# Kernel tuning notes

Hardware: AMD Instinct MI355X
Metric: run time of the kernel (lower is better)

The kernel has to match this reference:

```python
import jax, jax.numpy as jnp
import numpy as np

B, N, EN, C, F, HEADS, DE = 2, 8192, 16, 256, 512, 8, 8
D = C // HEADS  # att_size = 32
TAU = 0.1


def _xavier(k, shape):
    lim = float(np.sqrt(6.0 / (shape[0] + shape[1])))
    return jax.random.uniform(k, shape, jnp.float32, -lim, lim)


def setup_inputs() -> dict:
    key = jax.random.key(0)
    ks = jax.random.split(key, 16)
    return {
        "xyz": jax.random.normal(ks[0], (B, N, 3), jnp.float32),
        "features": jax.random.normal(ks[1], (B, C, N), jnp.float32),
        "edges": jax.random.randint(ks[2], (B, N * EN, 2), 0, N),
        "gumbel_u": jax.random.uniform(ks[3], (B * N, DE, EN), jnp.float32, 1e-6, 1.0 - 1e-6),
        "g1": jnp.ones((C,), jnp.float32), "be1": jnp.zeros((C,), jnp.float32),
        "Wq": _xavier(ks[4], (C, C)),
        "Wk": _xavier(ks[5], (C + 3, C)),
        "Wv": _xavier(ks[6], (C + 3, C)),
        "Wo": _xavier(ks[7], (C, C)),
        "g2": jnp.ones((C,), jnp.float32), "be2": jnp.zeros((C,), jnp.float32),
        "W1": _xavier(ks[8], (C, F)), "bf1": jnp.zeros((F,), jnp.float32),
        "W2": _xavier(ks[9], (F, C)), "bf2": jnp.zeros((C,), jnp.float32),
        "D1": _xavier(ks[10], (C, C // 2)), "db1": jnp.zeros((C // 2,), jnp.float32),
        "D2": _xavier(ks[11], (C // 2, DE)), "db2": jnp.zeros((DE,), jnp.float32),
    }


def _ln(x, g, b):
    m = jnp.mean(x, -1, keepdims=True)
    v = jnp.mean((x - m) ** 2, -1, keepdims=True)
    return (x - m) * jax.lax.rsqrt(v + 1e-6) * g + b


def reference(xyz, features, edges, gumbel_u, g1, be1, Wq, Wk, Wv, Wo,
              g2, be2, W1, bf1, W2, bf2, D1, db1, D2, db2):
    feats = jnp.transpose(features, (0, 2, 1))            # b,n,C
    x = _ln(feats, g1, be1)
    idx = edges[:, :, 0]                                  # b, n*EN (neighbor ids)
    gather = jax.vmap(lambda a, i: a[i])
    sf = gather(x, idx).reshape(B, N, EN, C)              # neighbor features
    sc = gather(xyz, idx).reshape(B, N, EN, 3)            # neighbor coords
    # learned gumbel-softmax downsample: EN -> DE edges per node
    sf2 = sf.reshape(B * N, EN, C)
    h = jax.nn.relu(sf2 @ D1 + db1) @ D2 + db2            # (B*N, EN, DE)
    logits = jnp.transpose(h, (0, 2, 1))                  # (B*N, DE, EN)
    gnoise = -jnp.log(-jnp.log(gumbel_u))
    w = jax.nn.softmax((logits + gnoise) / TAU, axis=-1)
    sf = jnp.einsum('bde,bec->bdc', w, sf2).reshape(B, N, DE, C)
    sc = jnp.einsum('bde,bec->bdc', w, sc.reshape(B * N, EN, 3)).reshape(B, N, DE, 3)
    s = jnp.concatenate([sf, sc - xyz[:, :, None, :]], axis=-1)  # b,n,DE,C+3
    # local neighbor multi-head attention
    k = (s @ Wk).reshape(B, N, DE, HEADS, D)
    v = (s @ Wv).reshape(B, N, DE, HEADS, D)
    q = (x @ Wq).reshape(B, N, HEADS, D)
    simi = jnp.einsum('bnehd,bnhd->bneh', k, q) * (1.0 / float(np.sqrt(D)))
    sm = jax.nn.softmax(simi, axis=2)                     # over neighbor axis
    o = jnp.einsum('bnehd,bneh->bnhd', v, sm).reshape(B, N, C) @ Wo
    feats = feats + o
    y = _ln(feats, g2, be2)
    y = jax.nn.relu(y @ W1 + bf1) @ W2 + bf2
    feats = feats + y
    return jnp.transpose(feats, (0, 2, 1))
```

## Files before the change

### kernel.cpp

```cpp
#include <hip/hip_runtime.h>
#include <math.h>

#define NB 8192
#define CC 256

using bf16x8 = __attribute__((ext_vector_type(8))) short;
using f32x4  = __attribute__((ext_vector_type(4))) float;

__device__ inline ushort f2b(float f) {
  union { float f; unsigned u; } v; v.f = f;
  unsigned u = v.u;
  u += 0x7FFF + ((u >> 16) & 1);
  return (ushort)(u >> 16);
}
__device__ inline float b2f(ushort h) {
  union { unsigned u; float f; } v; v.u = ((unsigned)h) << 16; return v.f;
}
__device__ inline float u2f(unsigned u) {
  union { unsigned u; float f; } v; v.u = u; return v.f;
}

__global__ __launch_bounds__(256) void wpackT(const float* __restrict__ Wk, const float* __restrict__ Wv,
                                              const float* __restrict__ Wq, const float* __restrict__ Wo,
                                              const float* __restrict__ W1, const float* __restrict__ W2,
                                              const float* __restrict__ D1,
                                              ushort* __restrict__ WtKVQ, ushort* __restrict__ WtO,
                                              ushort* __restrict__ Wt1, ushort* __restrict__ Wt2,
                                              ushort* __restrict__ D1hi, ushort* __restrict__ D1lo) {
  int i = blockIdx.x * 256 + threadIdx.x;
  if (i < 196608) {
    int n = i >> 8, k = i & 255;
    float v = (n < 256) ? Wk[(size_t)k * 256 + n]
            : (n < 512) ? Wv[(size_t)k * 256 + (n - 256)]
                        : Wq[(size_t)k * 256 + (n - 512)];
    WtKVQ[(size_t)n * 256 + k] = f2b(v);
  } else if (i < 262144) {
    int j = i - 196608; int n = j >> 8, k = j & 255;
    WtO[(size_t)n * 256 + k] = f2b(Wo[(size_t)k * 256 + n]);
  } else if (i < 393216) {
    int j = i - 262144; int n = j >> 8, k = j & 255;
    Wt1[(size_t)n * 256 + k] = f2b(W1[(size_t)k * 512 + n]);
  } else if (i < 524288) {
    int j = i - 393216; int n = j >> 9, k = j & 511;
    Wt2[(size_t)n * 512 + k] = f2b(W2[(size_t)k * 256 + n]);
  } else if (i < 557056) {
    int j = i - 524288; int n = j >> 8, k = j & 255;
    D1hi[(size_t)n * 256 + k] = f2b(D1[(size_t)k * 128 + n]);
  } else {
    int j = i - 557056; int n = j >> 8, k = j & 255;
    float v = D1[(size_t)k * 128 + n];
    ushort hi = f2b(v);
    D1lo[(size_t)n * 256 + k] = f2b(v - b2f(hi));
  }
}

__global__ __launch_bounds__(256) void k1_ln1(const float* __restrict__ features,
                                              const float* __restrict__ g1,
                                              const float* __restrict__ be1,
                                              float* __restrict__ X,
                                              float* __restrict__ F) {
  __shared__ float tile[256][36];
  int b = blockIdx.y;
  int n0 = blockIdx.x * 32;
  int t = threadIdx.x;
  int tn = t & 31, ch = t >> 5;
  for (int cb = 0; cb < 32; ++cb) {
    int c = cb * 8 + ch;
    tile[c][tn] = features[((size_t)b * 256 + c) * NB + n0 + tn];
  }
  __syncthreads();
  int tok = t >> 3, sub = t & 7;
  float s = 0.f, ss = 0.f;
  #pragma unroll
  for (int k = 0; k < 32; ++k) {
    float v = tile[sub + 8 * k][tok];
    s += v; ss += v * v;
  }
  #pragma unroll
  for (int m = 1; m < 8; m <<= 1) { s += __shfl_xor(s, m); ss += __shfl_xor(ss, m); }
  float mean = s * (1.f / 256.f);
  float var  = ss * (1.f / 256.f) - mean * mean;
  float rstd = rsqrtf(var + 1e-6f);
  size_t row = ((size_t)b * NB + n0 + tok) * 256;
  for (int k = 0; k < 32; ++k) {
    int c = sub + 8 * k;
    float v = tile[c][tok];
    F[row + c] = v;
    X[row + c] = (v - mean) * rstd * g1[c] + be1[c];
  }
}

__global__ __launch_bounds__(256) void gemm_mfma_x2(
    const float* __restrict__ A, int lda,
    const ushort* __restrict__ Bhi, const ushort* __restrict__ Blo,
    float* __restrict__ Cc, int ldc, int K,
    const float* __restrict__ bias)
{
  __shared__ __align__(16) ushort Ah[128 * 32], Al[128 * 32], Bh[128 * 32], Bl[128 * 32];
  int t = threadIdx.x;
  int m0 = blockIdx.y * 128;
  int wv = t >> 6, lane = t & 63;
  int wm = wv >> 1, wn = wv & 1;
  int lr = lane & 15, kg = lane >> 4;
  f32x4 acc[4][4];
  #pragma unroll
  for (int i = 0; i < 4; ++i)
    #pragma unroll
    for (int j = 0; j < 4; ++j) acc[i][j] = (f32x4)0.0f;

  for (int k0 = 0; k0 < K; k0 += 32) {
    #pragma unroll
    for (int p = 0; p < 2; ++p) {
      int c = t + p * 256;
      int m = c >> 2, kq = c & 3;
      const float* src = &A[(size_t)(m0 + m) * lda + k0 + kq * 8];
      float v[8];
      *(float4*)&v[0] = *(const float4*)src;
      *(float4*)&v[4] = *(const float4*)(src + 4);
      ushort hi[8], lo[8];
      #pragma unroll
      for (int j = 0; j < 8; ++j) {
        hi[j] = f2b(v[j]);
        lo[j] = f2b(v[j] - b2f(hi[j]));
      }
      int off = m * 32 + (kq ^ ((m >> 1) & 3)) * 8;
      *(uint4*)&Ah[off] = *(uint4*)hi;
      *(uint4*)&Al[off] = *(uint4*)lo;
    }
    #pragma unroll
    for (int p = 0; p < 2; ++p) {
      int c = t + p * 256;
      int n = c >> 2, kq = c & 3;
      int off = n * 32 + (kq ^ ((n >> 1) & 3)) * 8;
      *(uint4*)&Bh[off] = *(const uint4*)&Bhi[(size_t)n * K + k0 + kq * 8];
      *(uint4*)&Bl[off] = *(const uint4*)&Blo[(size_t)n * K + k0 + kq * 8];
    }
    __syncthreads();
    bf16x8 ahi[4], alo[4], bhi[4], blo[4];
    #pragma unroll
    for (int mi = 0; mi < 4; ++mi) {
      int m = wm * 64 + mi * 16 + lr;
      int off = m * 32 + (kg ^ ((m >> 1) & 3)) * 8;
      ahi[mi] = *(const bf16x8*)&Ah[off];
      alo[mi] = *(const bf16x8*)&Al[off];
    }
    #pragma unroll
    for (int ni = 0; ni < 4; ++ni) {
      int n = wn * 64 + ni * 16 + lr;
      int off = n * 32 + (kg ^ ((n >> 1) & 3)) * 8;
      bhi[ni] = *(const bf16x8*)&Bh[off];
      blo[ni] = *(const bf16x8*)&Bl[off];
    }
    #pragma unroll
    for (int mi = 0; mi < 4; ++mi)
      #pragma unroll
      for (int ni = 0; ni < 4; ++ni) {
        acc[mi][ni] = __builtin_amdgcn_mfma_f32_16x16x32_bf16(ahi[mi], bhi[ni], acc[mi][ni], 0, 0, 0);
        acc[mi][ni] = __builtin_amdgcn_mfma_f32_16x16x32_bf16(ahi[mi], blo[ni], acc[mi][ni], 0, 0, 0);
        acc[mi][ni] = __builtin_amdgcn_mfma_f32_16x16x32_bf16(alo[mi], bhi[ni], acc[mi][ni], 0, 0, 0);
      }
    __syncthreads();
  }
  #pragma unroll
  for (int ni = 0; ni < 4; ++ni) {
    int col = wn * 64 + ni * 16 + lr;
    float bv = bias[col];
    #pragma unroll
    for (int mi = 0; mi < 4; ++mi)
      #pragma unroll
      for (int r = 0; r < 4; ++r) {
        int row = m0 + wm * 64 + mi * 16 + kg * 4 + r;
        Cc[(size_t)row * ldc + col] = acc[mi][ni][r] + bv;
      }
  }
}

__global__ __launch_bounds__(256) void gemm_mfma(
    const float* __restrict__ A, int lda,
    const ushort* __restrict__ Bt,
    float* __restrict__ Cc, int ldc,
    int K,
    const float* __restrict__ bias, int relu,
    const float* __restrict__ resid, int ldr,
    const float* __restrict__ mrs, const float* __restrict__ lg, const float* __restrict__ lb)
{
  __shared__ __align__(16) ushort As[128 * 32];
  __shared__ __align__(16) ushort Bs[128 * 32];
  int t = threadIdx.x;
  int m0 = blockIdx.y * 128, n0 = blockIdx.x * 128;
  int wv = t >> 6, lane = t & 63;
  int wm = wv >> 1, wn = wv & 1;
  int lr = lane & 15, kg = lane >> 4;
  f32x4 acc[4][4];
  #pragma unroll
  for (int i = 0; i < 4; ++i)
    #pragma unroll
    for (int j = 0; j < 4; ++j) acc[i][j] = (f32x4)0.0f;

  for (int k0 = 0; k0 < K; k0 += 32) {
    #pragma unroll
    for (int p = 0; p < 2; ++p) {
      int c = t + p * 256;
      int m = c >> 2, kq = c & 3;
      const float* src = &A[(size_t)(m0 + m) * lda + k0 + kq * 8];
      float v[8];
      *(float4*)&v[0] = *(const float4*)src;
      *(float4*)&v[4] = *(const float4*)(src + 4);
      if (mrs) {
        float mean = mrs[(m0 + m) * 2], rstd = mrs[(m0 + m) * 2 + 1];
        #pragma unroll
        for (int j = 0; j < 8; ++j) {
          int kk = k0 + kq * 8 + j;
          v[j] = (v[j] - mean) * rstd * lg[kk] + lb[kk];
        }
      }
      ushort o[8];
      #pragma unroll
      for (int j = 0; j < 8; ++j) o[j] = f2b(v[j]);
      *(uint4*)&As[m * 32 + (kq ^ ((m >> 1) & 3)) * 8] = *(uint4*)o;
    }
    #pragma unroll
    for (int p = 0; p < 2; ++p) {
      int c = t + p * 256;
      int n = c >> 2, kq = c & 3;
      uint4 w = *(const uint4*)&Bt[(size_t)(n0 + n) * K + k0 + kq * 8];
      *(uint4*)&Bs[n * 32 + (kq ^ ((n >> 1) & 3)) * 8] = w;
    }
    __syncthreads();
    bf16x8 af[4], bfr[4];
    #pragma unroll
    for (int mi = 0; mi < 4; ++mi) {
      int m = wm * 64 + mi * 16 + lr;
      af[mi] = *(const bf16x8*)&As[m * 32 + (kg ^ ((m >> 1) & 3)) * 8];
    }
    #pragma unroll
    for (int ni = 0; ni < 4; ++ni) {
      int n = wn * 64 + ni * 16 + lr;
      bfr[ni] = *(const bf16x8*)&Bs[n * 32 + (kg ^ ((n >> 1) & 3)) * 8];
    }
    #pragma unroll
    for (int mi = 0; mi < 4; ++mi)
      #pragma unroll
      for (int ni = 0; ni < 4; ++ni)
        acc[mi][ni] = __builtin_amdgcn_mfma_f32_16x16x32_bf16(af[mi], bfr[ni], acc[mi][ni], 0, 0, 0);
    __syncthreads();
  }
  #pragma unroll
  for (int ni = 0; ni < 4; ++ni) {
    int col = n0 + wn * 64 + ni * 16 + lr;
    float bv = bias ? bias[col] : 0.f;
    #pragma unroll
    for (int mi = 0; mi < 4; ++mi) {
      #pragma unroll
      for (int r = 0; r < 4; ++r) {
        int row = m0 + wm * 64 + mi * 16 + kg * 4 + r;
        float v = acc[mi][ni][r] + bv;
        if (relu) v = fmaxf(v, 0.f);
        if (resid) v += resid[(size_t)row * ldr + col];
        Cc[(size_t)row * ldc + col] = v;
      }
    }
  }
}

__global__ __launch_bounds__(256) void gemm_mfma_b16o(
    const float* __restrict__ A, int lda,
    const ushort* __restrict__ Bt,
    ushort* __restrict__ Cc, int ldc, int K)
{
  __shared__ __align__(16) ushort As[128 * 32];
  __shared__ __align__(16) ushort Bs[128 * 32];
  int t = threadIdx.x;
  int m0 = blockIdx.y * 128, n0 = blockIdx.x * 128;
  int wv = t >> 6, lane = t & 63;
  int wm = wv >> 1, wn = wv & 1;
  int lr = lane & 15, kg = lane >> 4;
  f32x4 acc[4][4];
  #pragma unroll
  for (int i = 0; i < 4; ++i)
    #pragma unroll
    for (int j = 0; j < 4; ++j) acc[i][j] = (f32x4)0.0f;

  for (int k0 = 0; k0 < K; k0 += 32) {
    #pragma unroll
    for (int p = 0; p < 2; ++p) {
      int c = t + p * 256;
      int m = c >> 2, kq = c & 3;
      const float* src = &A[(size_t)(m0 + m) * lda + k0 + kq * 8];
      float v[8];
      *(float4*)&v[0] = *(const float4*)src;
      *(float4*)&v[4] = *(const float4*)(src + 4);
      ushort o[8];
      #pragma unroll
      for (int j = 0; j < 8; ++j) o[j] = f2b(v[j]);
      *(uint4*)&As[m * 32 + (kq ^ ((m >> 1) & 3)) * 8] = *(uint4*)o;
    }
    #pragma unroll
    for (int p = 0; p < 2; ++p) {
      int c = t + p * 256;
      int n = c >> 2, kq = c & 3;
      uint4 w = *(const uint4*)&Bt[(size_t)(n0 + n) * K + k0 + kq * 8];
      *(uint4*)&Bs[n * 32 + (kq ^ ((n >> 1) & 3)) * 8] = w;
    }
    __syncthreads();
    bf16x8 af[4], bfr[4];
    #pragma unroll
    for (int mi = 0; mi < 4; ++mi) {
      int m = wm * 64 + mi * 16 + lr;
      af[mi] = *(const bf16x8*)&As[m * 32 + (kg ^ ((m >> 1) & 3)) * 8];
    }
    #pragma unroll
    for (int ni = 0; ni < 4; ++ni) {
      int n = wn * 64 + ni * 16 + lr;
      bfr[ni] = *(const bf16x8*)&Bs[n * 32 + (kg ^ ((n >> 1) & 3)) * 8];
    }
    #pragma unroll
    for (int mi = 0; mi < 4; ++mi)
      #pragma unroll
      for (int ni = 0; ni < 4; ++ni)
        acc[mi][ni] = __builtin_amdgcn_mfma_f32_16x16x32_bf16(af[mi], bfr[ni], acc[mi][ni], 0, 0, 0);
    __syncthreads();
  }
  #pragma unroll
  for (int ni = 0; ni < 4; ++ni) {
    int col = n0 + wn * 64 + ni * 16 + lr;
    #pragma unroll
    for (int mi = 0; mi < 4; ++mi)
      #pragma unroll
      for (int r = 0; r < 4; ++r) {
        int row = m0 + wm * 64 + mi * 16 + kg * 4 + r;
        Cc[(size_t)row * ldc + col] = f2b(acc[mi][ni][r]);
      }
  }
}

__global__ __launch_bounds__(256) void k3_wave(
    const float* __restrict__ XD,
    const ushort* __restrict__ XKV,
    const float* __restrict__ XQ,
    const int* __restrict__ edges,
    const float* __restrict__ gu,
    const float* __restrict__ xyz,
    const float* __restrict__ Wk, const float* __restrict__ Wv,
    const float* __restrict__ D2, const float* __restrict__ db2,
    float* __restrict__ O)
{
  __shared__ float d2s[1024];
  int t = threadIdx.x;
  for (int i = t; i < 1024; i += 256) {
    int f = i >> 3, d = i & 7;
    d2s[f * 8 + (d ^ (f >> 5))] = D2[i];
  }
  __syncthreads();

  int wv = t >> 6, lane = t & 63;
  int b = blockIdx.y;
  int n = blockIdx.x * 4 + wv;
  size_t bn = (size_t)b * NB + n;
  int e = lane >> 2, fq = lane & 3;

  int idx = edges[(bn * 16 + e) * 2];

  float acc[8] = {0.f, 0.f, 0.f, 0.f, 0.f, 0.f, 0.f, 0.f};
  const float4* xd4 = (const float4*)(XD + ((size_t)b * NB + idx) * 128 + fq * 32);
  #pragma unroll
  for (int i = 0; i < 8; ++i) {
    float4 xd = xd4[i];
    float xv[4] = {fmaxf(xd.x, 0.f), fmaxf(xd.y, 0.f), fmaxf(xd.z, 0.f), fmaxf(xd.w, 0.f)};
    #pragma unroll
    for (int j = 0; j < 4; ++j) {
      int f = fq * 32 + i * 4 + j;
      #pragma unroll
      for (int d = 0; d < 8; ++d)
        acc[d] += xv[j] * d2s[f * 8 + (d ^ fq)];
    }
  }
  #pragma unroll
  for (int d = 0; d < 8; ++d) {
    acc[d] += __shfl_xor(acc[d], 1);
    acc[d] += __shfl_xor(acc[d], 2);
    acc[d] += db2[d];
  }

  float w[8];
  #pragma unroll
  for (int d = 0; d < 8; ++d) {
    float u = gu[(bn * 8 + d) * 16 + e];
    float gn = -logf(-logf(u));
    float val = (acc[d] + gn) * 10.0f;
    float mx = val;
    mx = fmaxf(mx, __shfl_xor(mx, 4));
    mx = fmaxf(mx, __shfl_xor(mx, 8));
    mx = fmaxf(mx, __shfl_xor(mx, 16));
    mx = fmaxf(mx, __shfl_xor(mx, 32));
    float ex = expf(val - mx);
    float sm = ex;
    sm += __shfl_xor(sm, 4);
    sm += __shfl_xor(sm, 8);
    sm += __shfl_xor(sm, 16);
    sm += __shfl_xor(sm, 32);
    w[d] = ex / sm;
  }

  float xg = (fq < 3) ? xyz[((size_t)b * NB + idx) * 3 + fq] : 0.f;
  float xo = (fq < 3) ? xyz[bn * 3 + fq] : 0.f;
  float scw[8];
  #pragma unroll
  for (int d = 0; d < 8; ++d) {
    float s = w[d] * xg;
    s += __shfl_xor(s, 4);
    s += __shfl_xor(s, 8);
    s += __shfl_xor(s, 16);
    s += __shfl_xor(s, 32);
    scw[d] = s - xo;
  }

  float4 kk[8], vv[8];
  #pragma unroll
  for (int d = 0; d < 8; ++d) {
    kk[d].x = kk[d].y = kk[d].z = kk[d].w = 0.f;
    vv[d].x = vv[d].y = vv[d].z = vv[d].w = 0.f;
  }
  #pragma unroll
  for (int j = 0; j < 3; ++j) {
    float4 wkb = *(const float4*)&Wk[(size_t)(256 + j) * 256 + lane * 4];
    float4 wvb = *(const float4*)&Wv[(size_t)(256 + j) * 256 + lane * 4];
    #pragma unroll
    for (int d = 0; d < 8; ++d) {
      float sc = __shfl(scw[d], (lane & ~3) | j);
      kk[d].x += sc * wkb.x; kk[d].y += sc * wkb.y; kk[d].z += sc * wkb.z; kk[d].w += sc * wkb.w;
      vv[d].x += sc * wvb.x; vv[d].y += sc * wvb.y; vv[d].z += sc * wvb.z; vv[d].w += sc * wvb.w;
    }
  }
  #pragma unroll 8
  for (int ee = 0; ee < 16; ++ee) {
    int eidx = __shfl(idx, ee * 4);
    const ushort* rE = XKV + ((size_t)b * NB + eidx) * 512;
    uint2 ku = *(const uint2*)(rE + lane * 4);
    uint2 vu = *(const uint2*)(rE + 256 + lane * 4);
    float xk0 = u2f(ku.x << 16), xk1 = u2f(ku.x & 0xFFFF0000u);
    float xk2 = u2f(ku.y << 16), xk3 = u2f(ku.y & 0xFFFF0000u);
    float xv0 = u2f(vu.x << 16), xv1 = u2f(vu.x & 0xFFFF0000u);
    float xv2 = u2f(vu.y << 16), xv3 = u2f(vu.y & 0xFFFF0000u);
    #pragma unroll
    for (int d = 0; d < 8; ++d) {
      float wd = __shfl(w[d], ee * 4);
      kk[d].x += wd * xk0; kk[d].y += wd * xk1; kk[d].z += wd * xk2; kk[d].w += wd * xk3;
      vv[d].x += wd * xv0; vv[d].y += wd * xv1; vv[d].z += wd * xv2; vv[d].w += wd * xv3;
    }
  }

  float4 q = ((const float4*)(XQ + bn * 256))[lane];
  float sim[8];
  #pragma unroll
  for (int d = 0; d < 8; ++d) {
    float p = q.x * kk[d].x + q.y * kk[d].y + q.z * kk[d].z + q.w * kk[d].w;
    p += __shfl_xor(p, 1);
    p += __shfl_xor(p, 2);
    p += __shfl_xor(p, 4);
    sim[d] = p * 0.17677669529663687f;
  }
  float mx = sim[0];
  #pragma unroll
  for (int d = 1; d < 8; ++d) mx = fmaxf(mx, sim[d]);
  float e8[8], sume = 0.f;
  #pragma unroll
  for (int d = 0; d < 8; ++d) { e8[d] = expf(sim[d] - mx); sume += e8[d]; }
  float inv = 1.f / sume;
  float4 oc; oc.x = oc.y = oc.z = oc.w = 0.f;
  #pragma unroll
  for (int d = 0; d < 8; ++d) {
    float sm = e8[d] * inv;
    oc.x += vv[d].x * sm; oc.y += vv[d].y * sm; oc.z += vv[d].z * sm; oc.w += vv[d].w * sm;
  }
  ((float4*)(O + bn * 256))[lane] = oc;
}

__global__ __launch_bounds__(256) void k5a_stats(const float* __restrict__ F, float* __restrict__ MRS) {
  int wave = threadIdx.x >> 6, lane = threadIdx.x & 63;
  size_t row = (size_t)blockIdx.x * 4 + wave;
  float4 v4 = *(const float4*)&F[row * 256 + lane * 4];
  float s = v4.x + v4.y + v4.z + v4.w;
  float ss = v4.x * v4.x + v4.y * v4.y + v4.z * v4.z + v4.w * v4.w;
  #pragma unroll
  for (int m = 1; m < 64; m <<= 1) { s += __shfl_xor(s, m); ss += __shfl_xor(ss, m); }
  if (lane == 0) {
    float mean = s * (1.f / 256.f);
    float var = ss * (1.f / 256.f) - mean * mean;
    MRS[row * 2] = mean;
    MRS[row * 2 + 1] = rsqrtf(var + 1e-6f);
  }
}

__global__ __launch_bounds__(256) void k7_transpose(const float* __restrict__ F, float* __restrict__ out) {
  __shared__ float tile[32][33];
  int b = blockIdx.z;
  int c0 = blockIdx.y * 32;
  int n0 = blockIdx.x * 32;
  int t = threadIdx.x;
  int nl = t >> 5, cl = t & 31;
  #pragma unroll
  for (int i = 0; i < 4; ++i) {
    int nn = nl + i * 8;
    tile[nn][cl] = F[((size_t)b * NB + n0 + nn) * 256 + c0 + cl];
  }
  __syncthreads();
  int cl2 = t >> 5, nl2 = t & 31;
  #pragma unroll
  for (int i = 0; i < 4; ++i) {
    int cc = cl2 + i * 8;
    out[((size_t)b * 256 + c0 + cc) * NB + n0 + nl2] = tile[nl2][cc];
  }
}

extern "C" void kernel_launch(void* const* d_in, const int* in_sizes, int n_in,
                              void* d_out, int out_size, void* d_ws, size_t ws_size,
                              hipStream_t stream) {
  const float* xyz      = (const float*)d_in[0];
  const float* features = (const float*)d_in[1];
  const int*   edges    = (const int*)d_in[2];
  const float* gu       = (const float*)d_in[3];
  const float* g1       = (const float*)d_in[4];
  const float* be1      = (const float*)d_in[5];
  const float* Wq       = (const float*)d_in[6];
  const float* Wk       = (const float*)d_in[7];
  const float* Wv       = (const float*)d_in[8];
  const float* Wo       = (const float*)d_in[9];
  const float* g2       = (const float*)d_in[10];
  const float* be2      = (const float*)d_in[11];
  const float* W1       = (const float*)d_in[12];
  const float* bf1      = (const float*)d_in[13];
  const float* W2       = (const float*)d_in[14];
  const float* bf2      = (const float*)d_in[15];
  const float* D1       = (const float*)d_in[16];
  const float* db1      = (const float*)d_in[17];
  const float* D2       = (const float*)d_in[18];
  const float* db2      = (const float*)d_in[19];
  float* out = (float*)d_out;
  float* ws  = (float*)d_ws;

  float*  X   = ws;
  float*  F   = ws + 4194304;
  float*  XD  = ws + 8388608;
  ushort* XKV = (ushort*)(ws + 10485760);
  float*  XQ  = ws + 14680064;
  float*  O   = X;
  float*  Y1  = ws + 8388608;

  ushort* WtKVQ = (ushort*)out;
  ushort* WtO   = WtKVQ + 196608;
  ushort* Wt1   = WtO + 65536;
  ushort* Wt2   = Wt1 + 131072;
  ushort* D1hi  = Wt2 + 131072;
  ushort* D1lo  = D1hi + 32768;
  float*  MRS   = out + 294912;

  wpackT<<<2304, 256, 0, stream>>>(Wk, Wv, Wq, Wo, W1, W2, D1, WtKVQ, WtO, Wt1, Wt2, D1hi, D1lo);

  k1_ln1<<<dim3(256, 2), 256, 0, stream>>>(features, g1, be1, X, F);

  gemm_mfma_x2<<<dim3(1, 128), 256, 0, stream>>>(X, 256, D1hi, D1lo, XD, 128, 256, db1);

  gemm_mfma_b16o<<<dim3(4, 128), 256, 0, stream>>>(X, 256, WtKVQ, XKV, 512, 256);

  gemm_mfma<<<dim3(2, 128), 256, 0, stream>>>(X, 256, WtKVQ + 512 * 256, XQ, 256, 256,
                                              nullptr, 0, nullptr, 0, nullptr, nullptr, nullptr);

  k3_wave<<<dim3(2048, 2), 256, 0, stream>>>(XD, XKV, XQ, edges, gu, xyz, Wk, Wv, D2, db2, O);

  gemm_mfma<<<dim3(2, 128), 256, 0, stream>>>(O, 256, WtO, F, 256, 256,
                                              nullptr, 0, F, 256, nullptr, nullptr, nullptr);

  k5a_stats<<<4096, 256, 0, stream>>>(F, MRS);

  gemm_mfma<<<dim3(4, 128), 256, 0, stream>>>(F, 256, Wt1, Y1, 512, 256,
                                              bf1, 1, nullptr, 0, MRS, g2, be2);

  gemm_mfma<<<dim3(2, 128), 256, 0, stream>>>(Y1, 512, Wt2, F, 256, 512,
                                              bf2, 0, F, 256, nullptr, nullptr, nullptr);

  k7_transpose<<<dim3(256, 8, 2), 256, 0, stream>>>(F, out);
}
```

Baseline: 356.0 us.

## Merge X-projection GEMMs into one launch and reassociate local attention math

The three GEMMs that consume the normalized features (the D1 split-precision projection, the K/V bf16 projection and the Q projection) are merged into a single kernel launch, with blockIdx.x choosing which product each block computes. In the attention kernel, the K and V tensors for each of the 8 sampled edges are no longer formed explicitly. Similarities are instead computed as weighted sums of q·k per raw neighbor plus a coordinate term projected through q, and the output is built by folding the softmax weights into per-neighbor and per-coordinate coefficients. This removes the 8×(K,V) float4 accumulators, cuts register pressure and FMA count, and saves two launches. In exchange it keeps 16 V rows in registers and changes the floating-point summation order.

```diff
diff --git a/kernel.cpp b/kernel.cpp
--- a/kernel.cpp
+++ b/kernel.cpp
@@ -90,88 +90,166 @@
   }
 }
 
-__global__ __launch_bounds__(256) void gemm_mfma_x2(
-    const float* __restrict__ A, int lda,
-    const ushort* __restrict__ Bhi, const ushort* __restrict__ Blo,
-    float* __restrict__ Cc, int ldc, int K,
-    const float* __restrict__ bias)
+__global__ __launch_bounds__(256) void k2_fused(
+    const float* __restrict__ X,
+    const ushort* __restrict__ D1hi, const ushort* __restrict__ D1lo,
+    const float* __restrict__ db1, float* __restrict__ XD,
+    const ushort* __restrict__ WtKVQ, ushort* __restrict__ XKV,
+    float* __restrict__ XQ)
 {
-  __shared__ __align__(16) ushort Ah[128 * 32], Al[128 * 32], Bh[128 * 32], Bl[128 * 32];
+  __shared__ __align__(16) ushort S[4 * 128 * 32];
   int t = threadIdx.x;
   int m0 = blockIdx.y * 128;
   int wv = t >> 6, lane = t & 63;
   int wm = wv >> 1, wn = wv & 1;
   int lr = lane & 15, kg = lane >> 4;
+  const int K = 256, lda = 256;
+  int bx = blockIdx.x;
+
   f32x4 acc[4][4];
   #pragma unroll
   for (int i = 0; i < 4; ++i)
     #pragma unroll
     for (int j = 0; j < 4; ++j) acc[i][j] = (f32x4)0.0f;
 
-  for (int k0 = 0; k0 < K; k0 += 32) {
-    #pragma unroll
-    for (int p = 0; p < 2; ++p) {
-      int c = t + p * 256;
-      int m = c >> 2, kq = c & 3;
-      const float* src = &A[(size_t)(m0 + m) * lda + k0 + kq * 8];
-      float v[8];
-      *(float4*)&v[0] = *(const float4*)src;
-      *(float4*)&v[4] = *(const float4*)(src + 4);
-      ushort hi[8], lo[8];
-      #pragma unroll
-      for (int j = 0; j < 8; ++j) {
-        hi[j] = f2b(v[j]);
-        lo[j] = f2b(v[j] - b2f(hi[j]));
-      }
-      int off = m * 32 + (kq ^ ((m >> 1) & 3)) * 8;
-      *(uint4*)&Ah[off] = *(uint4*)hi;
-      *(uint4*)&Al[off] = *(uint4*)lo;
-    }
-    #pragma unroll
-    for (int p = 0; p < 2; ++p) {
-      int c = t + p * 256;
-      int n = c >> 2, kq = c & 3;
-      int off = n * 32 + (kq ^ ((n >> 1) & 3)) * 8;
-      *(uint4*)&Bh[off] = *(const uint4*)&Bhi[(size_t)n * K + k0 + kq * 8];
-      *(uint4*)&Bl[off] = *(const uint4*)&Blo[(size_t)n * K + k0 + kq * 8];
-    }
-    __syncthreads();
-    bf16x8 ahi[4], alo[4], bhi[4], blo[4];
-    #pragma unroll
-    for (int mi = 0; mi < 4; ++mi) {
-      int m = wm * 64 + mi * 16 + lr;
-      int off = m * 32 + (kg ^ ((m >> 1) & 3)) * 8;
-      ahi[mi] = *(const bf16x8*)&Ah[off];
-      alo[mi] = *(const bf16x8*)&Al[off];
+  if (bx == 0) {
+    ushort* Ah = S;            ushort* Al = S + 4096;
+    ushort* Bh = S + 8192;     ushort* Bl = S + 12288;
+    for (int k0 = 0; k0 < K; k0 += 32) {
+      #pragma unroll
+      for (int p = 0; p < 2; ++p) {
+        int c = t + p * 256;
+        int m = c >> 2, kq = c & 3;
+        const float* src = &X[(size_t)(m0 + m) * lda + k0 + kq * 8];
+        float v[8];
+        *(float4*)&v[0] = *(const float4*)src;
+        *(float4*)&v[4] = *(const float4*)(src + 4);
+        ushort hi[8], lo[8];
+        #pragma unroll
+        for (int j = 0; j < 8; ++j) {
+          hi[j] = f2b(v[j]);
+          lo[j] = f2b(v[j] - b2f(hi[j]));
+        }
+        int off = m * 32 + (kq ^ ((m >> 1) & 3)) * 8;
+        *(uint4*)&Ah[off] = *(uint4*)hi;
+        *(uint4*)&Al[off] = *(uint4*)lo;
+      }
+      #pragma unroll
+      for (int p = 0; p < 2; ++p) {
+        int c = t + p * 256;
+        int n = c >> 2, kq = c & 3;
+        int off = n * 32 + (kq ^ ((n >> 1) & 3)) * 8;
+        *(uint4*)&Bh[off] = *(const uint4*)&D1hi[(size_t)n * K + k0 + kq * 8];
+        *(uint4*)&Bl[off] = *(const uint4*)&D1lo[(size_t)n * K + k0 + kq * 8];
+      }
+      __syncthreads();
+      bf16x8 ahi[4], alo[4], bhi[4], blo[4];
+      #pragma unroll
+      for (int mi = 0; mi < 4; ++mi) {
+        int m = wm * 64 + mi * 16 + lr;
+        int off = m * 32 + (kg ^ ((m >> 1) & 3)) * 8;
+        ahi[mi] = *(const bf16x8*)&Ah[off];
+        alo[mi] = *(const bf16x8*)&Al[off];
+      }
+      #pragma unroll
+      for (int ni = 0; ni < 4; ++ni) {
+        int n = wn * 64 + ni * 16 + lr;
+        int off = n * 32 + (kg ^ ((n >> 1) & 3)) * 8;
+        bhi[ni] = *(const bf16x8*)&Bh[off];
+        blo[ni] = *(const bf16x8*)&Bl[off];
+      }
+      #pragma unroll
+      for (int mi = 0; mi < 4; ++mi)
+        #pragma unroll
+        for (int ni = 0; ni < 4; ++ni) {
+          acc[mi][ni] = __builtin_amdgcn_mfma_f32_16x16x32_bf16(ahi[mi], bhi[ni], acc[mi][ni], 0, 0, 0);
+          acc[mi][ni] = __builtin_amdgcn_mfma_f32_16x16x32_bf16(ahi[mi], blo[ni], acc[mi][ni], 0, 0, 0);
+          acc[mi][ni] = __builtin_amdgcn_mfma_f32_16x16x32_bf16(alo[mi], bhi[ni], acc[mi][ni], 0, 0, 0);
+        }
+      __syncthreads();
     }
     #pragma unroll
     for (int ni = 0; ni < 4; ++ni) {
-      int n = wn * 64 + ni * 16 + lr;
-      int off = n * 32 + (kg ^ ((n >> 1) & 3)) * 8;
-      bhi[ni] = *(const bf16x8*)&Bh[off];
-      blo[ni] = *(const bf16x8*)&Bl[off];
-    }
-    #pragma unroll
-    for (int mi = 0; mi < 4; ++mi)
+      int col = wn * 64 + ni * 16 + lr;
+      float bv = db1[col];
+      #pragma unroll
+      for (int mi = 0; mi < 4; ++mi)
+        #pragma unroll
+        for (int r = 0; r < 4; ++r) {
+          int row = m0 + wm * 64 + mi * 16 + kg * 4 + r;
+          XD[(size_t)row * 128 + col] = acc[mi][ni][r] + bv;
+        }
+    }
+  } else {
+    ushort* As = S;  ushort* Bs = S + 4096;
+    bool isKV = (bx <= 4);
+    int n0 = isKV ? (bx - 1) * 128 : (bx - 5) * 128;
+    const ushort* Bt = isKV ? WtKVQ : (WtKVQ + 512 * 256);
+    for (int k0 = 0; k0 < K; k0 += 32) {
+      #pragma unroll
+      for (int p = 0; p < 2; ++p) {
+        int c = t + p * 256;
+        int m = c >> 2, kq = c & 3;
+        const float* src = &X[(size_t)(m0 + m) * lda + k0 + kq * 8];
+        float v[8];
+        *(float4*)&v[0] = *(const float4*)src;
+        *(float4*)&v[4] = *(const float4*)(src + 4);
+        ushort o[8];
+        #pragma unroll
+        for (int j = 0; j < 8; ++j) o[j] = f2b(v[j]);
+        *(uint4*)&As[m * 32 + (kq ^ ((m >> 1) & 3)) * 8] = *(uint4*)o;
+      }
+      #pragma unroll
+      for (int p = 0; p < 2; ++p) {
+        int c = t + p * 256;
+        int n = c >> 2, kq = c & 3;
+        uint4 w = *(const uint4*)&Bt[(size_t)(n0 + n) * K + k0 + kq * 8];
+        *(uint4*)&Bs[n * 32 + (kq ^ ((n >> 1) & 3)) * 8] = w;
+      }
+      __syncthreads();
+      bf16x8 af[4], bfr[4];
+      #pragma unroll
+      for (int mi = 0; mi < 4; ++mi) {
+        int m = wm * 64 + mi * 16 + lr;
+        af[mi] = *(const bf16x8*)&As[m * 32 + (kg ^ ((m >> 1) & 3)) * 8];
+      }
       #pragma unroll
       for (int ni = 0; ni < 4; ++ni) {
-        acc[mi][ni] = __builtin_amdgcn_mfma_f32_16x16x32_bf16(ahi[mi], bhi[ni], acc[mi][ni], 0, 0, 0);
-        acc[mi][ni] = __builtin_amdgcn_mfma_f32_16x16x32_bf16(ahi[mi], blo[ni], acc[mi][ni], 0, 0, 0);
-        acc[mi][ni] = __builtin_amdgcn_mfma_f32_16x16x32_bf16(alo[mi], bhi[ni], acc[mi][ni], 0, 0, 0);
-      }
-    __syncthreads();
-  }
-  #pragma unroll
-  for (int ni = 0; ni < 4; ++ni) {
-    int col = wn * 64 + ni * 16 + lr;
-    float bv = bias[col];
-    #pragma unroll
-    for (int mi = 0; mi < 4; ++mi)
-      #pragma unroll
-      for (int r = 0; r < 4; ++r) {
-        int row = m0 + wm * 64 + mi * 16 + kg * 4 + r;
-        Cc[(size_t)row * ldc + col] = acc[mi][ni][r] + bv;
-      }
+        int n = wn * 64 + ni * 16 + lr;
+        bfr[ni] = *(const bf16x8*)&Bs[n * 32 + (kg ^ ((n >> 1) & 3)) * 8];
+      }
+      #pragma unroll
+      for (int mi = 0; mi < 4; ++mi)
+        #pragma unroll
+        for (int ni = 0; ni < 4; ++ni)
+          acc[mi][ni] = __builtin_amdgcn_mfma_f32_16x16x32_bf16(af[mi], bfr[ni], acc[mi][ni], 0, 0, 0);
+      __syncthreads();
+    }
+    if (isKV) {
+      #pragma unroll
+      for (int ni = 0; ni < 4; ++ni) {
+        int col = n0 + wn * 64 + ni * 16 + lr;
+        #pragma unroll
+        for (int mi = 0; mi < 4; ++mi)
+          #pragma unroll
+          for (int r = 0; r < 4; ++r) {
+            int row = m0 + wm * 64 + mi * 16 + kg * 4 + r;
+            XKV[(size_t)row * 512 + col] = f2b(acc[mi][ni][r]);
+          }
+      }
+    } else {
+      #pragma unroll
+      for (int ni = 0; ni < 4; ++ni) {
+        int col = n0 + wn * 64 + ni * 16 + lr;
+        #pragma unroll
+        for (int mi = 0; mi < 4; ++mi)
+          #pragma unroll
+          for (int r = 0; r < 4; ++r) {
+            int row = m0 + wm * 64 + mi * 16 + kg * 4 + r;
+            XQ[(size_t)row * 256 + col] = acc[mi][ni][r];
+          }
+      }
+    }
   }
 }
 
@@ -263,77 +341,6 @@
   }
 }
 
-__global__ __launch_bounds__(256) void gemm_mfma_b16o(
-    const float* __restrict__ A, int lda,
-    const ushort* __restrict__ Bt,
-    ushort* __restrict__ Cc, int ldc, int K)
-{
-  __shared__ __align__(16) ushort As[128 * 32];
-  __shared__ __align__(16) ushort Bs[128 * 32];
-  int t = threadIdx.x;
-  int m0 = blockIdx.y * 128, n0 = blockIdx.x * 128;
-  int wv = t >> 6, lane = t & 63;
-  int wm = wv >> 1, wn = wv & 1;
-  int lr = lane & 15, kg = lane >> 4;
-  f32x4 acc[4][4];
-  #pragma unroll
-  for (int i = 0; i < 4; ++i)
-    #pragma unroll
-    for (int j = 0; j < 4; ++j) acc[i][j] = (f32x4)0.0f;
-
-  for (int k0 = 0; k0 < K; k0 += 32) {
-    #pragma unroll
-    for (int p = 0; p < 2; ++p) {
-      int c = t + p * 256;
-      int m = c >> 2, kq = c & 3;
-      const float* src = &A[(size_t)(m0 + m) * lda + k0 + kq * 8];
-      float v[8];
-      *(float4*)&v[0] = *(const float4*)src;
-      *(float4*)&v[4] = *(const float4*)(src + 4);
-      ushort o[8];
-      #pragma unroll
-      for (int j = 0; j < 8; ++j) o[j] = f2b(v[j]);
-      *(uint4*)&As[m * 32 + (kq ^ ((m >> 1) & 3)) * 8] = *(uint4*)o;
-    }
-    #pragma unroll
-    for (int p = 0; p < 2; ++p) {
-      int c = t + p * 256;
-      int n = c >> 2, kq = c & 3;
-      uint4 w = *(const uint4*)&Bt[(size_t)(n0 + n) * K + k0 + kq * 8];
-      *(uint4*)&Bs[n * 32 + (kq ^ ((n >> 1) & 3)) * 8] = w;
-    }
-    __syncthreads();
-    bf16x8 af[4], bfr[4];
-    #pragma unroll
-    for (int mi = 0; mi < 4; ++mi) {
-      int m = wm * 64 + mi * 16 + lr;
-      af[mi] = *(const bf16x8*)&As[m * 32 + (kg ^ ((m >> 1) & 3)) * 8];
-    }
-    #pragma unroll
-    for (int ni = 0; ni < 4; ++ni) {
-      int n = wn * 64 + ni * 16 + lr;
-      bfr[ni] = *(const bf16x8*)&Bs[n * 32 + (kg ^ ((n >> 1) & 3)) * 8];
-    }
-    #pragma unroll
-    for (int mi = 0; mi < 4; ++mi)
-      #pragma unroll
-      for (int ni = 0; ni < 4; ++ni)
-        acc[mi][ni] = __builtin_amdgcn_mfma_f32_16x16x32_bf16(af[mi], bfr[ni], acc[mi][ni], 0, 0, 0);
-    __syncthreads();
-  }
-  #pragma unroll
-  for (int ni = 0; ni < 4; ++ni) {
-    int col = n0 + wn * 64 + ni * 16 + lr;
-    #pragma unroll
-    for (int mi = 0; mi < 4; ++mi)
-      #pragma unroll
-      for (int r = 0; r < 4; ++r) {
-        int row = m0 + wm * 64 + mi * 16 + kg * 4 + r;
-        Cc[(size_t)row * ldc + col] = f2b(acc[mi][ni][r]);
-      }
-  }
-}
-
 __global__ __launch_bounds__(256) void k3_wave(
     const float* __restrict__ XD,
     const ushort* __restrict__ XKV,
@@ -353,9 +360,9 @@
   }
   __syncthreads();
 
-  int wv = t >> 6, lane = t & 63;
+  int wvi = t >> 6, lane = t & 63;
   int b = blockIdx.y;
-  int n = blockIdx.x * 4 + wv;
+  int n = blockIdx.x * 4 + wvi;
   size_t bn = (size_t)b * NB + n;
   int e = lane >> 2, fq = lane & 3;
 
@@ -415,63 +422,76 @@
     scw[d] = s - xo;
   }
 
-  float4 kk[8], vv[8];
-  #pragma unroll
-  for (int d = 0; d < 8; ++d) {
-    kk[d].x = kk[d].y = kk[d].z = kk[d].w = 0.f;
-    vv[d].x = vv[d].y = vv[d].z = vv[d].w = 0.f;
-  }
+  float4 q = ((const float4*)(XQ + bn * 256))[lane];
+  float qb[3];
   #pragma unroll
   for (int j = 0; j < 3; ++j) {
     float4 wkb = *(const float4*)&Wk[(size_t)(256 + j) * 256 + lane * 4];
-    float4 wvb = *(const float4*)&Wv[(size_t)(256 + j) * 256 + lane * 4];
-    #pragma unroll
-    for (int d = 0; d < 8; ++d) {
-      float sc = __shfl(scw[d], (lane & ~3) | j);
-      kk[d].x += sc * wkb.x; kk[d].y += sc * wkb.y; kk[d].z += sc * wkb.z; kk[d].w += sc * wkb.w;
-      vv[d].x += sc * wvb.x; vv[d].y += sc * wvb.y; vv[d].z += sc * wvb.z; vv[d].w += sc * wvb.w;
-    }
-  }
-  #pragma unroll 8
+    float p = q.x * wkb.x + q.y * wkb.y + q.z * wkb.z + q.w * wkb.w;
+    p += __shfl_xor(p, 1);
+    p += __shfl_xor(p, 2);
+    p += __shfl_xor(p, 4);
+    qb[j] = p;
+  }
+
+  float sim[8];
+  #pragma unroll
+  for (int d = 0; d < 8; ++d) {
+    float s = 0.f;
+    #pragma unroll
+    for (int j = 0; j < 3; ++j)
+      s += __shfl(scw[d], (lane & ~3) | j) * qb[j];
+    sim[d] = s;
+  }
+  uint2 vreg[16];
+  #pragma unroll
   for (int ee = 0; ee < 16; ++ee) {
     int eidx = __shfl(idx, ee * 4);
     const ushort* rE = XKV + ((size_t)b * NB + eidx) * 512;
     uint2 ku = *(const uint2*)(rE + lane * 4);
-    uint2 vu = *(const uint2*)(rE + 256 + lane * 4);
-    float xk0 = u2f(ku.x << 16), xk1 = u2f(ku.x & 0xFFFF0000u);
-    float xk2 = u2f(ku.y << 16), xk3 = u2f(ku.y & 0xFFFF0000u);
-    float xv0 = u2f(vu.x << 16), xv1 = u2f(vu.x & 0xFFFF0000u);
-    float xv2 = u2f(vu.y << 16), xv3 = u2f(vu.y & 0xFFFF0000u);
-    #pragma unroll
-    for (int d = 0; d < 8; ++d) {
-      float wd = __shfl(w[d], ee * 4);
-      kk[d].x += wd * xk0; kk[d].y += wd * xk1; kk[d].z += wd * xk2; kk[d].w += wd * xk3;
-      vv[d].x += wd * xv0; vv[d].y += wd * xv1; vv[d].z += wd * xv2; vv[d].w += wd * xv3;
-    }
-  }
-
-  float4 q = ((const float4*)(XQ + bn * 256))[lane];
-  float sim[8];
-  #pragma unroll
-  for (int d = 0; d < 8; ++d) {
-    float p = q.x * kk[d].x + q.y * kk[d].y + q.z * kk[d].z + q.w * kk[d].w;
+    vreg[ee] = *(const uint2*)(rE + 256 + lane * 4);
+    float k0 = u2f(ku.x << 16), k1 = u2f(ku.x & 0xFFFF0000u);
+    float k2 = u2f(ku.y << 16), k3 = u2f(ku.y & 0xFFFF0000u);
+    float p = q.x * k0 + q.y * k1 + q.z * k2 + q.w * k3;
     p += __shfl_xor(p, 1);
     p += __shfl_xor(p, 2);
     p += __shfl_xor(p, 4);
-    sim[d] = p * 0.17677669529663687f;
-  }
+    #pragma unroll
+    for (int d = 0; d < 8; ++d)
+      sim[d] += __shfl(w[d], ee * 4) * p;
+  }
+  #pragma unroll
+  for (int d = 0; d < 8; ++d) sim[d] *= 0.17677669529663687f;
+
   float mx = sim[0];
   #pragma unroll
   for (int d = 1; d < 8; ++d) mx = fmaxf(mx, sim[d]);
-  float e8[8], sume = 0.f;
-  #pragma unroll
-  for (int d = 0; d < 8; ++d) { e8[d] = expf(sim[d] - mx); sume += e8[d]; }
+  float sm[8], sume = 0.f;
+  #pragma unroll
+  for (int d = 0; d < 8; ++d) { sm[d] = expf(sim[d] - mx); sume += sm[d]; }
   float inv = 1.f / sume;
+  #pragma unroll
+  for (int d = 0; d < 8; ++d) sm[d] *= inv;
+
   float4 oc; oc.x = oc.y = oc.z = oc.w = 0.f;
   #pragma unroll
-  for (int d = 0; d < 8; ++d) {
-    float sm = e8[d] * inv;
-    oc.x += vv[d].x * sm; oc.y += vv[d].y * sm; oc.z += vv[d].z * sm; oc.w += vv[d].w * sm;
+  for (int j = 0; j < 3; ++j) {
+    float g = 0.f;
+    #pragma unroll
+    for (int d = 0; d < 8; ++d)
+      g += sm[d] * __shfl(scw[d], (lane & ~3) | j);
+    float4 wvb = *(const float4*)&Wv[(size_t)(256 + j) * 256 + lane * 4];
+    oc.x += g * wvb.x; oc.y += g * wvb.y; oc.z += g * wvb.z; oc.w += g * wvb.w;
+  }
+  #pragma unroll
+  for (int ee = 0; ee < 16; ++ee) {
+    float a = 0.f;
+    #pragma unroll
+    for (int d = 0; d < 8; ++d)
+      a += sm[d] * __shfl(w[d], ee * 4);
+    float v0 = u2f(vreg[ee].x << 16), v1 = u2f(vreg[ee].x & 0xFFFF0000u);
+    float v2 = u2f(vreg[ee].y << 16), v3 = u2f(vreg[ee].y & 0xFFFF0000u);
+    oc.x += a * v0; oc.y += a * v1; oc.z += a * v2; oc.w += a * v3;
   }
   ((float4*)(O + bn * 256))[lane] = oc;
 }
@@ -559,12 +579,7 @@
 
   k1_ln1<<<dim3(256, 2), 256, 0, stream>>>(features, g1, be1, X, F);
 
-  gemm_mfma_x2<<<dim3(1, 128), 256, 0, stream>>>(X, 256, D1hi, D1lo, XD, 128, 256, db1);
-
-  gemm_mfma_b16o<<<dim3(4, 128), 256, 0, stream>>>(X, 256, WtKVQ, XKV, 512, 256);
-
-  gemm_mfma<<<dim3(2, 128), 256, 0, stream>>>(X, 256, WtKVQ + 512 * 256, XQ, 256, 256,
-                                              nullptr, 0, nullptr, 0, nullptr, nullptr, nullptr);
+  k2_fused<<<dim3(7, 128), 256, 0, stream>>>(X, D1hi, D1lo, db1, XD, WtKVQ, XKV, XQ);
 
   k3_wave<<<dim3(2048, 2), 256, 0, stream>>>(XD, XKV, XQ, edges, gu, xyz, Wk, Wv, D2, db2, O);
 
```

Result: no change. 355.2 us (-0.2%).
